# Performance work log

Hardware: AMD Instinct MI355X
Metric: run time of the kernel (lower is better)

Reference implementation:

```python
import jax, jax.numpy as jnp
import numpy as np


def _conv(x, w, b):
    # NCHW conv, 5x5, stride 1, SAME (pad 2)
    y = jax.lax.conv_general_dilated(x, w, (1, 1), 'SAME',
                                     dimension_numbers=('NCHW', 'OIHW', 'NCHW'))
    return y + b[None, :, None, None]


def _fwd(sequence_output, attention, adjacency, mention_idx, link_start, node_types, hts,
         W_trans, b_trans, type_embed, W_rel, W_self, b_rgcn,
         conv1_w, conv1_b, conv2_w, conv2_b, conv3_w, conv3_b,
         ht_W, ht_b, bil_W, bil_b):
    B, c, _ = sequence_output.shape
    E, M, LS = 22, 3, 16
    seq = sequence_output @ W_trans + b_trans              # [B,c,512] extractor_trans
    att_mean = attention.mean(1)                           # [B,c,c] head-averaged
    # ---- link nodes: attention-weighted span average (mean over heads, then matmul, then mean) ----
    pos = link_start[:, :, None] + jnp.arange(LS)          # [B,L,LS]
    fp = pos.reshape(B, -1)
    span = jnp.take_along_axis(seq, fp[:, :, None], axis=1).reshape(B, -1, LS, seq.shape[-1])
    rows = jnp.take_along_axis(att_mean, fp[:, :, None], axis=1).reshape(B, -1, LS, c)
    A = jnp.take_along_axis(rows, pos[:, :, None, :], axis=3)   # [B,L,LS,LS]
    link_nodes = jnp.einsum('blij,bljd->blid', A, span).mean(2)  # [B,L,512]
    # ---- mention gather + per-entity logsumexp pooling ----
    mf = mention_idx.reshape(B, -1)                              # [B,E*M]
    m_emb = jnp.take_along_axis(seq, mf[:, :, None], axis=1)     # [B,EM,512]
    entity_nodes = jax.nn.logsumexp(m_emb.reshape(B, E, M, -1), axis=2)   # [B,E,512]
    att_rows = jnp.take_along_axis(attention, mf[:, None, :, None], axis=2)  # [B,h,EM,c]
    entity_att = att_rows.reshape(B, att_rows.shape[1], E, M, c).mean(3)     # [B,h,E,c]
    # ---- assemble graph nodes + type embedding ----
    nodes = jnp.concatenate([entity_nodes, m_emb, link_nodes], axis=1)       # [B,N,512]
    nodes = jnp.concatenate([nodes, type_embed[node_types]], axis=-1)        # [B,N,532]
    # ---- 1-layer RGCN, 4 relations, row-normalized adjacency ----
    adj_n = adjacency / (adjacency.sum(-1, keepdims=True) + 1e-5)
    msg = jnp.einsum('brij,bjd->brid', adj_n, nodes)
    gcn = jax.nn.relu(jnp.einsum('brid,rdk->bik', msg, W_rel) + nodes @ W_self + b_rgcn)
    ent = gcn[:, :E]                                             # [B,E,512]
    # ---- entity context: normalized head-mean attention @ seq ----
    ea = entity_att.mean(1)
    ea = ea / (ea.sum(-1, keepdims=True) + 1e-5)
    e_ctx = jnp.einsum('bec,bcd->bed', ea, seq)                  # [B,E,512]
    # ---- per-channel outer-product relation maps ('ij,jk->jik') -> conv reasoning ----
    x = jnp.einsum('bid,bkd->bdik', ent, ent) + jnp.einsum('bid,bkd->bdik', e_ctx, e_ctx)
    x = jax.nn.relu(_conv(x, conv1_w, conv1_b))
    x = jax.nn.relu(_conv(x, conv2_w, conv2_b))
    x = jax.nn.relu(_conv(x, conv3_w, conv3_b))                  # [B,512,E,E]
    # ---- head/tail pair classification ----
    hi, ti = hts[..., 0], hts[..., 1]
    hs = jnp.take_along_axis(ent, hi[:, :, None], axis=1)
    ts = jnp.take_along_axis(ent, ti[:, :, None], axis=1)
    mflat = x.transpose(0, 2, 3, 1).reshape(B, E * E, -1)
    mfe = jnp.take_along_axis(mflat, (hi * E + ti)[:, :, None], axis=1)
    feat = jnp.concatenate([hs, ts, mfe, hs * ts], axis=-1)      # [B,P,2048]
    ht = jnp.tanh(feat @ ht_W + ht_b)                            # [B,P,1024]
    return ht @ bil_W + bil_b                                    # [B,P,97]


def setup_inputs() -> dict:
    key = jax.random.key(0)
    ks = jax.random.split(key, 16)
    B, c, H, h = 4, 1024, 768, 12
    E, M, L, N, P = 22, 3, 30, 118, 462
    emb, ic = 512, 256
    s = lambda k, sh: jax.random.normal(k, sh, jnp.float32) * 0.02
    inp = {}
    inp['sequence_output'] = jax.random.normal(ks[0], (B, c, H), jnp.float32)
    inp['attention'] = jax.random.uniform(ks[1], (B, h, c, c), dtype=jnp.float32)
    inp['adjacency'] = jax.random.uniform(ks[2], (B, 4, N, N), dtype=jnp.float32)
    inp['mention_idx'] = jax.random.randint(ks[3], (B, E, M), 0, c)
    inp['link_start'] = jax.random.randint(ks[4], (B, L), 0, c - 16)
    inp['node_types'] = jax.random.randint(ks[5], (B, N), 0, 3)
    inp['hts'] = jax.random.randint(ks[6], (B, P, 2), 0, E)
    inp['W_trans'] = s(ks[7], (H, emb)); inp['b_trans'] = jnp.zeros((emb,), jnp.float32)
    inp['type_embed'] = s(ks[8], (3, 20))
    inp['W_rel'] = s(ks[9], (4, emb + 20, emb))
    inp['W_self'] = s(ks[10], (emb + 20, emb)); inp['b_rgcn'] = jnp.zeros((emb,), jnp.float32)
    inp['conv1_w'] = s(ks[11], (ic, emb, 5, 5)); inp['conv1_b'] = jnp.zeros((ic,), jnp.float32)
    inp['conv2_w'] = s(ks[12], (ic, ic, 5, 5)); inp['conv2_b'] = jnp.zeros((ic,), jnp.float32)
    inp['conv3_w'] = s(ks[13], (emb, ic, 5, 5)); inp['conv3_b'] = jnp.zeros((emb,), jnp.float32)
    inp['ht_W'] = s(ks[14], (emb * 4, emb * 2)); inp['ht_b'] = jnp.zeros((emb * 2,), jnp.float32)
    inp['bil_W'] = s(ks[15], (emb * 2, 97)); inp['bil_b'] = jnp.zeros((97,), jnp.float32)
    return inp


def reference(sequence_output, attention, adjacency, mention_idx, link_start, node_types, hts,
              W_trans, b_trans, type_embed, W_rel, W_self, b_rgcn,
              conv1_w, conv1_b, conv2_w, conv2_b, conv3_w, conv3_b,
              ht_W, ht_b, bil_W, bil_b):
    return _fwd(sequence_output, attention, adjacency, mention_idx, link_start, node_types, hts,
                W_trans, b_trans, type_embed, W_rel, W_self, b_rgcn,
                conv1_w, conv1_b, conv2_w, conv2_b, conv3_w, conv3_b,
                ht_W, ht_b, bil_W, bil_b)
```

## Files before the change

### kernel.cpp

```cpp
#include <hip/hip_runtime.h>
#include <hip/hip_bf16.h>

constexpr int B   = 4;
constexpr int C   = 1024;
constexpr int HH  = 768;
constexpr int NHD = 12;
constexpr int E   = 22;
constexpr int MM  = 3;
constexpr int LL  = 30;
constexpr int NN  = 118;
constexpr int PP  = 462;
constexpr int EMB = 512;
constexpr int IC  = 256;
constexpr int LS  = 16;
constexpr int ND  = 532;
constexpr int KCAT = 4*ND + ND;


__global__ __launch_bounds__(256) void att_mean4_kernel(const float4* __restrict__ att,
                                                        float4* __restrict__ out) {
    int idx = blockIdx.x * 256 + threadIdx.x;
    int tot = B * C * C / 4;
    if (idx >= tot) return;
    int b = idx / (C * C / 4), rc = idx % (C * C / 4);
    const float4* p = att + (size_t)b * NHD * (C * C / 4) + rc;
    float sx = 0.f, sy = 0.f, sz = 0.f, sw = 0.f;
#pragma unroll
    for (int hh = 0; hh < NHD; hh++) {
        float4 v = p[(size_t)hh * (C * C / 4)];
        sx += v.x; sy += v.y; sz += v.z; sw += v.w;
    }
    const float inv = 1.0f / NHD;
    float4 r; r.x = sx * inv; r.y = sy * inv; r.z = sz * inv; r.w = sw * inv;
    out[idx] = r;
}

__global__ __launch_bounds__(256) void gemm_kernel(const float* __restrict__ A,
                                                   const float* __restrict__ Bm,
                                                   const float* __restrict__ bias,
                                                   float* __restrict__ Cc,
                                                   int M, int N, int K, int act) {
    __shared__ __align__(16) float As[16][68];
    __shared__ __align__(16) float Bs[16][68];
    int tid = threadIdx.x;
    int tx = tid & 15, ty = tid >> 4;
    int row0 = blockIdx.y * 64, col0 = blockIdx.x * 64;
    float acc[4][4] = {};
    for (int k0 = 0; k0 < K; k0 += 16) {
#pragma unroll
        for (int pass = 0; pass < 4; pass++) {
            int r = pass * 16 + (tid >> 4);
            int gr = row0 + r, gk = k0 + (tid & 15);
            As[tid & 15][r] = (gr < M && gk < K) ? A[(size_t)gr * K + gk] : 0.f;
        }
#pragma unroll
        for (int pass = 0; pass < 4; pass++) {
            int kk = pass * 4 + (tid >> 6);
            int cc = tid & 63;
            int gk = k0 + kk, gc = col0 + cc;
            Bs[kk][cc] = (gk < K && gc < N) ? Bm[(size_t)gk * N + gc] : 0.f;
        }
        __syncthreads();
#pragma unroll
        for (int kk = 0; kk < 16; kk++) {
            float4 av = *(const float4*)&As[kk][ty * 4];
            float4 bv = *(const float4*)&Bs[kk][tx * 4];
            float a[4] = {av.x, av.y, av.z, av.w};
            float bb[4] = {bv.x, bv.y, bv.z, bv.w};
#pragma unroll
            for (int i = 0; i < 4; i++)
#pragma unroll
                for (int j = 0; j < 4; j++) acc[i][j] += a[i] * bb[j];
        }
        __syncthreads();
    }
#pragma unroll
    for (int i = 0; i < 4; i++) {
        int gr = row0 + ty * 4 + i;
        if (gr >= M) continue;
#pragma unroll
        for (int j = 0; j < 4; j++) {
            int gc = col0 + tx * 4 + j;
            if (gc >= N) continue;
            float v = acc[i][j] + (bias ? bias[gc] : 0.f);
            if (act == 1) v = fmaxf(v, 0.f);
            else if (act == 2) v = tanhf(v);
            Cc[(size_t)gr * N + gc] = v;
        }
    }
}

__global__ __launch_bounds__(256) void gemm_splitk_kernel(const float* __restrict__ A,
                                                          const float* __restrict__ Bm,
                                                          float* __restrict__ part,
                                                          int M, int N, int K, int kb) {
    __shared__ __align__(16) float As[16][68];
    __shared__ __align__(16) float Bs[16][68];
    int z = blockIdx.z;
    int kbeg = z * kb;
    int kend = (kbeg + kb < K) ? (kbeg + kb) : K;
    int tid = threadIdx.x;
    int tx = tid & 15, ty = tid >> 4;
    int row0 = blockIdx.y * 64, col0 = blockIdx.x * 64;
    float acc[4][4] = {};
    for (int k0 = kbeg; k0 < kend; k0 += 16) {
#pragma unroll
        for (int pass = 0; pass < 4; pass++) {
            int r = pass * 16 + (tid >> 4);
            int gr = row0 + r, gk = k0 + (tid & 15);
            As[tid & 15][r] = (gr < M && gk < kend) ? A[(size_t)gr * K + gk] : 0.f;
        }
#pragma unroll
        for (int pass = 0; pass < 4; pass++) {
            int kk = pass * 4 + (tid >> 6);
            int cc = tid & 63;
            int gk = k0 + kk, gc = col0 + cc;
            Bs[kk][cc] = (gk < kend && gc < N) ? Bm[(size_t)gk * N + gc] : 0.f;
        }
        __syncthreads();
#pragma unroll
        for (int kk = 0; kk < 16; kk++) {
            float4 av = *(const float4*)&As[kk][ty * 4];
            float4 bv = *(const float4*)&Bs[kk][tx * 4];
            float a[4] = {av.x, av.y, av.z, av.w};
            float bb[4] = {bv.x, bv.y, bv.z, bv.w};
#pragma unroll
            for (int i = 0; i < 4; i++)
#pragma unroll
                for (int j = 0; j < 4; j++) acc[i][j] += a[i] * bb[j];
        }
        __syncthreads();
    }
    float* dst = part + (size_t)z * M * N;
#pragma unroll
    for (int i = 0; i < 4; i++) {
        int gr = row0 + ty * 4 + i;
        if (gr >= M) continue;
#pragma unroll
        for (int j = 0; j < 4; j++) {
            int gc = col0 + tx * 4 + j;
            if (gc >= N) continue;
            dst[(size_t)gr * N + gc] = acc[i][j];
        }
    }
}

__global__ __launch_bounds__(256) void reduce_sba_kernel(const float* __restrict__ part,
                                                         const float* __restrict__ bias,
                                                         float* __restrict__ out,
                                                         int MN, int N, int S, int act) {
    int idx = blockIdx.x * 256 + threadIdx.x;
    if (idx >= MN) return;
    float s = bias[idx % N];
    for (int z = 0; z < S; z++) s += part[(size_t)z * MN + idx];
    if (act == 1) s = fmaxf(s, 0.f);
    out[idx] = s;
}

__global__ __launch_bounds__(256) void gemmb_kernel(const float* __restrict__ A0,
                                                    const float* __restrict__ B0,
                                                    float* __restrict__ C0,
                                                    int M, int N, int K,
                                                    long sA, long sB, long sC) {
    const float* A = A0 + (size_t)blockIdx.z * sA;
    const float* Bm = B0 + (size_t)blockIdx.z * sB;
    float* Cc = C0 + (size_t)blockIdx.z * sC;
    __shared__ __align__(16) float As[16][68];
    __shared__ __align__(16) float Bs[16][68];
    int tid = threadIdx.x;
    int tx = tid & 15, ty = tid >> 4;
    int row0 = blockIdx.y * 64, col0 = blockIdx.x * 64;
    float acc[4][4] = {};
    for (int k0 = 0; k0 < K; k0 += 16) {
#pragma unroll
        for (int pass = 0; pass < 4; pass++) {
            int r = pass * 16 + (tid >> 4);
            int gr = row0 + r, gk = k0 + (tid & 15);
            As[tid & 15][r] = (gr < M && gk < K) ? A[(size_t)gr * K + gk] : 0.f;
        }
#pragma unroll
        for (int pass = 0; pass < 4; pass++) {
            int kk = pass * 4 + (tid >> 6);
            int cc = tid & 63;
            int gk = k0 + kk, gc = col0 + cc;
            Bs[kk][cc] = (gk < K && gc < N) ? Bm[(size_t)gk * N + gc] : 0.f;
        }
        __syncthreads();
#pragma unroll
        for (int kk = 0; kk < 16; kk++) {
            float4 av = *(const float4*)&As[kk][ty * 4];
            float4 bv = *(const float4*)&Bs[kk][tx * 4];
            float a[4] = {av.x, av.y, av.z, av.w};
            float bb[4] = {bv.x, bv.y, bv.z, bv.w};
#pragma unroll
            for (int i = 0; i < 4; i++)
#pragma unroll
                for (int j = 0; j < 4; j++) acc[i][j] += a[i] * bb[j];
        }
        __syncthreads();
    }
#pragma unroll
    for (int i = 0; i < 4; i++) {
        int gr = row0 + ty * 4 + i;
        if (gr >= M) continue;
#pragma unroll
        for (int j = 0; j < 4; j++) {
            int gc = col0 + tx * 4 + j;
            if (gc >= N) continue;
            Cc[(size_t)gr * N + gc] = acc[i][j];
        }
    }
}

__global__ __launch_bounds__(256) void nodes_fill_kernel(const float* __restrict__ seq,
                                                         const int* __restrict__ mention_idx,
                                                         const int* __restrict__ node_types,
                                                         const float* __restrict__ type_embed,
                                                         float* __restrict__ nodes) {
    int n = blockIdx.x, b = blockIdx.y, t = threadIdx.x;
    float* dst = nodes + ((size_t)b * NN + n) * ND;
    if (n < E) {
        const int* mi = mention_idx + (b * E + n) * MM;
        int i0 = mi[0], i1 = mi[1], i2 = mi[2];
        const float* s0 = seq + ((size_t)b * C + i0) * EMB;
        const float* s1 = seq + ((size_t)b * C + i1) * EMB;
        const float* s2 = seq + ((size_t)b * C + i2) * EMB;
        for (int d = t; d < EMB; d += 256) {
            float v0 = s0[d], v1 = s1[d], v2 = s2[d];
            float mx = fmaxf(v0, fmaxf(v1, v2));
            dst[d] = mx + logf(expf(v0 - mx) + expf(v1 - mx) + expf(v2 - mx));
        }
    } else if (n < E + E * MM) {
        int m = n - E;
        int src = mention_idx[b * E * MM + m];
        const float* sp = seq + ((size_t)b * C + src) * EMB;
        for (int d = t; d < EMB; d += 256) dst[d] = sp[d];
    }
    if (t < 20) {
        int ty_ = node_types[b * NN + n];
        dst[EMB + t] = type_embed[ty_ * 20 + t];
    }
}

__global__ __launch_bounds__(256) void link_nodes_kernel(const float* __restrict__ seq,
                                                         const float* __restrict__ am,
                                                         const int* __restrict__ link_start,
                                                         float* __restrict__ nodes) {
    int l = blockIdx.x, b = blockIdx.y, t = threadIdx.x;
    __shared__ float Ash[LS][LS];
    __shared__ float w[LS];
    int start = link_start[b * LL + l];
    {
        int i = t >> 4, j = t & 15;
        Ash[i][j] = am[((size_t)b * C + start + i) * C + (start + j)];
    }
    __syncthreads();
    if (t < LS) {
        float s = 0.f;
#pragma unroll
        for (int i = 0; i < LS; i++) s += Ash[i][t];
        w[t] = s * (1.0f / LS);
    }
    __syncthreads();
    float* dst = nodes + ((size_t)b * NN + (E + E * MM) + l) * ND;
    for (int d = t; d < EMB; d += 256) {
        float acc = 0.f;
#pragma unroll
        for (int j = 0; j < LS; j++) acc += w[j] * seq[((size_t)b * C + start + j) * EMB + d];
        dst[d] = acc;
    }
}

__global__ __launch_bounds__(256) void ea_kernel(const float* __restrict__ am,
                                                 const int* __restrict__ mention_idx,
                                                 float* __restrict__ ea) {
    int e = blockIdx.x, b = blockIdx.y, t = threadIdx.x;
    const int* mi = mention_idx + (b * E + e) * MM;
    int i0 = mi[0], i1 = mi[1], i2 = mi[2];
    const float* r0 = am + ((size_t)b * C + i0) * C;
    const float* r1 = am + ((size_t)b * C + i1) * C;
    const float* r2 = am + ((size_t)b * C + i2) * C;
    float* dst = ea + ((size_t)b * E + e) * C;
    __shared__ float red[256];
    float psum = 0.f;
    for (int ct = t; ct < C; ct += 256) {
        float v = (r0[ct] + r1[ct] + r2[ct]) * (1.0f / 3.0f);
        dst[ct] = v;
        psum += v;
    }
    red[t] = psum;
    __syncthreads();
    for (int s = 128; s > 0; s >>= 1) {
        if (t < s) red[t] += red[t + s];
        __syncthreads();
    }
    float inv = 1.0f / (red[0] + 1e-5f);
    for (int ct = t; ct < C; ct += 256) dst[ct] *= inv;
}

__global__ __launch_bounds__(128) void adjn_kernel(const float* __restrict__ adj,
                                                   float* __restrict__ adjn) {
    int row = blockIdx.x;
    int t = threadIdx.x;
    const float* src = adj + (size_t)row * NN;
    __shared__ float red[128];
    float s = (t < NN) ? src[t] : 0.f;
    red[t] = s;
    __syncthreads();
    for (int st = 64; st > 0; st >>= 1) {
        if (t < st) red[t] += red[t + st];
        __syncthreads();
    }
    float inv = 1.0f / (red[0] + 1e-5f);
    if (t < NN) adjn[(size_t)row * NN + t] = src[t] * inv;
}

__global__ __launch_bounds__(256) void msg_kernel(const float* __restrict__ adjn,
                                                  const float* __restrict__ nodes,
                                                  float* __restrict__ Arow) {
    int i = blockIdx.x, r = blockIdx.y, b = blockIdx.z;
    int t = threadIdx.x;
    __shared__ float a_sh[NN];
    if (t < NN) a_sh[t] = adjn[(((size_t)b * 4 + r) * NN + i) * NN + t];
    __syncthreads();
    float* dst = Arow + ((size_t)b * NN + i) * KCAT;
    const float* nb = nodes + (size_t)b * NN * ND;
    for (int d = t; d < ND; d += 256) {
        float acc = 0.f;
        for (int j = 0; j < NN; j++) acc += a_sh[j] * nb[(size_t)j * ND + d];
        dst[r * ND + d] = acc;
        if (r == 0) dst[4 * ND + d] = nb[(size_t)i * ND + d];
    }
}

__global__ __launch_bounds__(512) void pairwise_kernel(const float* __restrict__ gcn,
                                                       const float* __restrict__ ectx,
                                                       float* __restrict__ x) {
    int d = blockIdx.x, b = blockIdx.y, t = threadIdx.x;
    __shared__ float ev[E], cv[E];
    if (t < E) ev[t] = gcn[((size_t)b * NN + t) * EMB + d];
    else if (t < 2 * E) cv[t - E] = ectx[((size_t)b * E + (t - E)) * EMB + d];
    __syncthreads();
    if (t < E * E) {
        int i = t / E, k = t % E;
        x[((size_t)b * EMB + d) * (E * E) + t] = ev[i] * ev[k] + cv[i] * cv[k];
    }
}

__global__ __launch_bounds__(256) void conv5k_kernel(const float* __restrict__ in,
                                                     const float* __restrict__ w,
                                                     float* __restrict__ part,
                                                     int Cin, int Cout, int CH) {
    constexpr int G = 2;
    int nch = Cin / CH;
    int z = blockIdx.z;
    int b = z / nch, ch = z - b * nch;
    int co0 = blockIdx.x * 64;
    int r0 = blockIdx.y * 8;
    int t = threadIdx.x;
    int tx = t & 15, ty = t >> 4;

    __shared__ __align__(16) float As[G * 25 * 68];
    __shared__ __align__(16) float Pl[G * 12 * 28];

    int qr[3], qc[3];
#pragma unroll
    for (int s = 0; s < 3; s++) {
        int q = tx + s * 16;
        qr[s] = q / 6;
        qc[s] = (q - qr[s] * 6) * 4;
    }

    float acc[3][4][4] = {};

    const float* inb = in + ((size_t)b * Cin + ch * CH) * 484;
    const float* wb  = w + ((size_t)co0 * Cin + (size_t)ch * CH) * 25;

    for (int c0 = 0; c0 < CH; c0 += G) {
        __syncthreads();
        for (int idx = t; idx < G * 336; idx += 256) {
            int g = idx / 336, rem = idx - g * 336;
            int r = rem / 28, c = rem - r * 28;
            int ih = r0 - 2 + r, iw = c - 2;
            float v = 0.f;
            if (ih >= 0 && ih < 22 && iw >= 0 && iw < 22)
                v = inb[(size_t)(c0 + g) * 484 + ih * 22 + iw];
            Pl[(g * 12 + r) * 28 + c] = v;
        }
        for (int idx = t; idx < G * 1600; idx += 256) {
            int g = idx / 1600, rem = idx - g * 1600;
            int co = rem / 25, tap = rem - co * 25;
            As[(g * 25 + tap) * 68 + co] = wb[(size_t)co * Cin * 25 + (size_t)(c0 + g) * 25 + tap];
        }
        __syncthreads();
#pragma unroll
        for (int g = 0; g < G; g++) {
            const float* plg = &Pl[g * 336];
            const float* asg = &As[g * 1700];
#pragma unroll
            for (int dy = 0; dy < 5; dy++) {
                float iv[3][8];
#pragma unroll
                for (int s = 0; s < 3; s++) {
                    float4 v0 = *(const float4*)&plg[(qr[s] + dy) * 28 + qc[s]];
                    float4 v1 = *(const float4*)&plg[(qr[s] + dy) * 28 + qc[s] + 4];
                    iv[s][0] = v0.x; iv[s][1] = v0.y; iv[s][2] = v0.z; iv[s][3] = v0.w;
                    iv[s][4] = v1.x; iv[s][5] = v1.y; iv[s][6] = v1.z; iv[s][7] = v1.w;
                }
#pragma unroll
                for (int dx = 0; dx < 5; dx++) {
                    float4 wv = *(const float4*)&asg[(dy * 5 + dx) * 68 + ty * 4];
                    float wf[4] = {wv.x, wv.y, wv.z, wv.w};
#pragma unroll
                    for (int s = 0; s < 3; s++)
#pragma unroll
                        for (int i = 0; i < 4; i++)
#pragma unroll
                            for (int j = 0; j < 4; j++)
                                acc[s][i][j] += wf[i] * iv[s][dx + j];
                }
            }
        }
    }
    float* dst0 = part + ((size_t)z * Cout + co0 + ty * 4) * 484;
#pragma unroll
    for (int s = 0; s < 3; s++) {
        int row = r0 + qr[s];
        if (row >= 22) continue;
#pragma unroll
        for (int i = 0; i < 4; i++) {
            float* dr = dst0 + (size_t)i * 484 + row * 22;
#pragma unroll
            for (int j = 0; j < 4; j++) {
                int col = qc[s] + j;
                if (col < 22) dr[col] = acc[s][i][j];
            }
        }
    }
}

__global__ __launch_bounds__(256) void reduce_bias_relu_kernel(const float* __restrict__ part,
                                                               const float* __restrict__ bias,
                                                               float* __restrict__ out,
                                                               int Cout, int nch) {
    int idx = blockIdx.x * 256 + threadIdx.x;
    int total = B * Cout * 484;
    if (idx >= total) return;
    int b = idx / (Cout * 484);
    int rem = idx % (Cout * 484);
    int co = rem / 484;
    float s = bias[co];
    const float* p = part + ((size_t)b * nch) * Cout * 484 + rem;
    for (int ch = 0; ch < nch; ch++) s += p[(size_t)ch * Cout * 484];
    out[idx] = fmaxf(s, 0.f);
}

__global__ __launch_bounds__(256) void reduce3_transpose_kernel(const float* __restrict__ part,
                                                                const float* __restrict__ bias,
                                                                float* __restrict__ mflat,
                                                                int nch) {
    __shared__ float tl[32][33];
    int b = blockIdx.z;
    int co0 = blockIdx.x * 32, pp0 = blockIdx.y * 32;
    int tx = threadIdx.x % 32, tyy = threadIdx.x / 32;
    for (int i = tyy; i < 32; i += 8) {
        int co = co0 + i, p = pp0 + tx;
        float v = 0.f;
        if (p < 484) {
            v = bias[co];
            const float* src = part + (((size_t)b * nch) * 512 + co) * 484 + p;
            for (int ch = 0; ch < nch; ch++) v += src[(size_t)ch * 512 * 484];
            v = fmaxf(v, 0.f);
        }
        tl[i][tx] = v;
    }
    __syncthreads();
    for (int i = tyy; i < 32; i += 8) {
        int p = pp0 + i, co = co0 + tx;
        if (p < 484) mflat[((size_t)b * 484 + p) * 512 + co] = tl[tx][i];
    }
}

__global__ __launch_bounds__(256) void feat_kernel(const float* __restrict__ gcn,
                                                   const float* __restrict__ mflat,
                                                   const int* __restrict__ hts,
                                                   float* __restrict__ feat) {
    int p = blockIdx.x, b = blockIdx.y, t = threadIdx.x;
    int hi = hts[((size_t)b * PP + p) * 2];
    int ti = hts[((size_t)b * PP + p) * 2 + 1];
    const float* hsrc = gcn + ((size_t)b * NN + hi) * EMB;
    const float* tsrc = gcn + ((size_t)b * NN + ti) * EMB;
    const float* msrc = mflat + ((size_t)b * 484 + hi * E + ti) * EMB;
    float* dst = feat + ((size_t)b * PP + p) * (4 * EMB);
    for (int d = t; d < EMB; d += 256) {
        float hv = hsrc[d], tv = tsrc[d];
        dst[d] = hv;
        dst[EMB + d] = tv;
        dst[2 * EMB + d] = msrc[d];
        dst[3 * EMB + d] = hv * tv;
    }
}

extern "C" void kernel_launch(void* const* d_in, const int* in_sizes, int n_in,
                              void* d_out, int out_size, void* d_ws, size_t ws_size,
                              hipStream_t stream) {
    const float* sequence_output = (const float*)d_in[0];
    const float* attention      = (const float*)d_in[1];
    const float* adjacency      = (const float*)d_in[2];
    const int*   mention_idx    = (const int*)d_in[3];
    const int*   link_start     = (const int*)d_in[4];
    const int*   node_types     = (const int*)d_in[5];
    const int*   hts            = (const int*)d_in[6];
    const float* W_trans        = (const float*)d_in[7];
    const float* b_trans        = (const float*)d_in[8];
    const float* type_embed     = (const float*)d_in[9];
    const float* W_rel          = (const float*)d_in[10];
    const float* W_self         = (const float*)d_in[11];
    const float* b_rgcn         = (const float*)d_in[12];
    const float* conv1_w        = (const float*)d_in[13];
    const float* conv1_b        = (const float*)d_in[14];
    const float* conv2_w        = (const float*)d_in[15];
    const float* conv2_b        = (const float*)d_in[16];
    const float* conv3_w        = (const float*)d_in[17];
    const float* conv3_b        = (const float*)d_in[18];
    const float* ht_W           = (const float*)d_in[19];
    const float* ht_b           = (const float*)d_in[20];
    const float* bil_W          = (const float*)d_in[21];
    const float* bil_b          = (const float*)d_in[22];
    float* out = (float*)d_out;
    float* ws = (float*)d_ws;

    float* att_mean = ws;
    float* Arow    = ws;
    float* Bcat    = ws + 1255520;
    float* gcnpart = ws + 2617440;
    float* xbuf    = ws;
    float* y1      = ws + 991232;
    float* y2      = ws + 1486848;
    float* part    = ws + 1982464;
    float* seqb    = ws + 4194304;
    float* ea      = ws + 6291456;
    float* mflat   = ws;
    float* feat    = ws + 991232;
    float* htbuf   = ws + 4800000;
    float* nodes   = ws + 9912320;
    float* adjn    = ws + 10163424;
    float* ectx    = ws + 10386208;
    float* gcnb    = ws + 10431264;

    att_mean4_kernel<<<(B * C * C / 4 + 255) / 256, 256, 0, stream>>>(
        (const float4*)attention, (float4*)att_mean);
    gemm_kernel<<<dim3(EMB / 64, (B * C) / 64), 256, 0, stream>>>(
        sequence_output, W_trans, b_trans, seqb, B * C, EMB, HH, 0);
    nodes_fill_kernel<<<dim3(NN, B), 256, 0, stream>>>(seqb, mention_idx, node_types,
                                                       type_embed, nodes);
    link_nodes_kernel<<<dim3(LL, B), 256, 0, stream>>>(seqb, att_mean, link_start, nodes);
    ea_kernel<<<dim3(E, B), 256, 0, stream>>>(att_mean, mention_idx, ea);
    gemmb_kernel<<<dim3(EMB / 64, 1, B), 256, 0, stream>>>(
        ea, seqb, ectx, E, EMB, C, (long)E * C, (long)C * EMB, (long)E * EMB);
    adjn_kernel<<<B * 4 * NN, 128, 0, stream>>>(adjacency, adjn);
    msg_kernel<<<dim3(NN, 4, B), 256, 0, stream>>>(adjn, nodes, Arow);
    hipMemcpyAsync(Bcat, W_rel, (size_t)4 * ND * EMB * sizeof(float),
                   hipMemcpyDeviceToDevice, stream);
    hipMemcpyAsync(Bcat + (size_t)4 * ND * EMB, W_self, (size_t)ND * EMB * sizeof(float),
                   hipMemcpyDeviceToDevice, stream);
    gemm_splitk_kernel<<<dim3(8, 8, 4), 256, 0, stream>>>(Arow, Bcat, gcnpart,
                                                          B * NN, EMB, KCAT, 672);
    reduce_sba_kernel<<<(B * NN * EMB + 255) / 256, 256, 0, stream>>>(
        gcnpart, b_rgcn, gcnb, B * NN * EMB, EMB, 4, 1);
    pairwise_kernel<<<dim3(EMB, B), 512, 0, stream>>>(gcnb, ectx, xbuf);
    conv5k_kernel<<<dim3(4, 3, B * 16), 256, 0, stream>>>(xbuf, conv1_w, part, 512, 256, 32);
    reduce_bias_relu_kernel<<<(B * 256 * 484 + 255) / 256, 256, 0, stream>>>(
        part, conv1_b, y1, 256, 16);
    conv5k_kernel<<<dim3(4, 3, B * 16), 256, 0, stream>>>(y1, conv2_w, part, 256, 256, 16);
    reduce_bias_relu_kernel<<<(B * 256 * 484 + 255) / 256, 256, 0, stream>>>(
        part, conv2_b, y2, 256, 16);
    conv5k_kernel<<<dim3(8, 3, B * 8), 256, 0, stream>>>(y2, conv3_w, part, 256, 512, 32);
    reduce3_transpose_kernel<<<dim3(16, 16, B), 256, 0, stream>>>(part, conv3_b, mflat, 8);
    feat_kernel<<<dim3(PP, B), 256, 0, stream>>>(gcnb, mflat, hts, feat);
    gemm_kernel<<<dim3(16, 29), 256, 0, stream>>>(feat, ht_W, ht_b, htbuf, B * PP, 1024,
                                                  2048, 2);
    gemm_kernel<<<dim3(2, 29), 256, 0, stream>>>(htbuf, bil_W, bil_b, out, B * PP, 97,
                                                 1024, 0);
}
```

Before: 2.240 ms.

## Run ht projection GEMM on bf16 MFMA with transposed bf16 weights

Casts the pair feature matrix to bf16 as it is built and transposes and converts ht_W to bf16 every call. The 1848x1024x2048 ht GEMM then runs on a new MFMA 16x16x32 bf16 kernel instead of the fp32 SIMT tiled GEMM. This is meant to cut the compute time of that GEMM and halve the bytes of its operands, at the cost of bf16 rounding error and an extra per-call transpose kernel.

```diff
diff --git a/kernel.cpp b/kernel.cpp
--- a/kernel.cpp
+++ b/kernel.cpp
@@ -15,6 +15,9 @@
 constexpr int LS  = 16;
 constexpr int ND  = 532;
 constexpr int KCAT = 4*ND + ND;
+
+typedef __attribute__((ext_vector_type(8))) short bf16x8;
+typedef __attribute__((ext_vector_type(4))) float f32x4;
 
 
 __global__ __launch_bounds__(256) void att_mean4_kernel(const float4* __restrict__ att,
@@ -208,6 +211,69 @@
             int gc = col0 + tx * 4 + j;
             if (gc >= N) continue;
             Cc[(size_t)gr * N + gc] = acc[i][j];
+        }
+    }
+}
+
+__global__ __launch_bounds__(256) void transpose_bf16_kernel(const float* __restrict__ W,
+                                                             __hip_bfloat16* __restrict__ Wt,
+                                                             int K, int N) {
+    __shared__ float tl[32][33];
+    int k0 = blockIdx.x * 32, n0 = blockIdx.y * 32;
+    int tx = threadIdx.x & 31, ty = threadIdx.x >> 5;
+    for (int i = ty; i < 32; i += 8) {
+        int k = k0 + i, n = n0 + tx;
+        tl[i][tx] = (k < K && n < N) ? W[(size_t)k * N + n] : 0.f;
+    }
+    __syncthreads();
+    for (int i = ty; i < 32; i += 8) {
+        int n = n0 + i, k = k0 + tx;
+        if (n < N && k < K) Wt[(size_t)n * K + k] = __float2bfloat16(tl[tx][i]);
+    }
+}
+
+__global__ __launch_bounds__(256) void gemm_mfma_kernel(const __hip_bfloat16* __restrict__ A,
+                                                        const __hip_bfloat16* __restrict__ Bt,
+                                                        const float* __restrict__ bias,
+                                                        float* __restrict__ Cc,
+                                                        int M, int N, int K, int act) {
+    __shared__ __align__(16) short Asub[4 * 64 * 8];
+    __shared__ __align__(16) short Bsub[4 * 64 * 8];
+    int t = threadIdx.x;
+    int row0 = blockIdx.y * 64, col0 = blockIdx.x * 64;
+    int w = t >> 6, l = t & 63;
+    int r = t >> 2, kh = t & 3;
+    f32x4 acc[4] = {};
+    for (int k0 = 0; k0 < K; k0 += 32) {
+        __syncthreads();
+        {
+            int gr = row0 + r;
+            uint4 va = make_uint4(0u, 0u, 0u, 0u);
+            if (gr < M) va = *(const uint4*)&A[(size_t)gr * K + k0 + kh * 8];
+            *(uint4*)&Asub[(kh * 64 + r) * 8] = va;
+            uint4 vb = *(const uint4*)&Bt[(size_t)(col0 + r) * K + k0 + kh * 8];
+            *(uint4*)&Bsub[(kh * 64 + r) * 8] = vb;
+        }
+        __syncthreads();
+        bf16x8 a = *(const bf16x8*)&Asub[((l >> 4) * 64 + w * 16 + (l & 15)) * 8];
+#pragma unroll
+        for (int n = 0; n < 4; n++) {
+            bf16x8 b = *(const bf16x8*)&Bsub[((l >> 4) * 64 + n * 16 + (l & 15)) * 8];
+            acc[n] = __builtin_amdgcn_mfma_f32_16x16x32_bf16(a, b, acc[n], 0, 0, 0);
+        }
+    }
+#pragma unroll
+    for (int n = 0; n < 4; n++) {
+        int col = col0 + n * 16 + (l & 15);
+        if (col >= N) continue;
+#pragma unroll
+        for (int i = 0; i < 4; i++) {
+            int row = row0 + w * 16 + (l >> 4) * 4 + i;
+            if (row >= M) continue;
+            float v = acc[n][i] + (bias ? bias[col] : 0.f);
+            if (act == 1) v = fmaxf(v, 0.f);
+            else if (act == 2) v = tanhf(v);
+            Cc[(size_t)row * N + col] = v;
         }
     }
 }
@@ -481,23 +547,23 @@
     }
 }
 
-__global__ __launch_bounds__(256) void feat_kernel(const float* __restrict__ gcn,
-                                                   const float* __restrict__ mflat,
-                                                   const int* __restrict__ hts,
-                                                   float* __restrict__ feat) {
+__global__ __launch_bounds__(256) void feat_bf16_kernel(const float* __restrict__ gcn,
+                                                        const float* __restrict__ mflat,
+                                                        const int* __restrict__ hts,
+                                                        __hip_bfloat16* __restrict__ feat) {
     int p = blockIdx.x, b = blockIdx.y, t = threadIdx.x;
     int hi = hts[((size_t)b * PP + p) * 2];
     int ti = hts[((size_t)b * PP + p) * 2 + 1];
     const float* hsrc = gcn + ((size_t)b * NN + hi) * EMB;
     const float* tsrc = gcn + ((size_t)b * NN + ti) * EMB;
     const float* msrc = mflat + ((size_t)b * 484 + hi * E + ti) * EMB;
-    float* dst = feat + ((size_t)b * PP + p) * (4 * EMB);
+    __hip_bfloat16* dst = feat + ((size_t)b * PP + p) * (4 * EMB);
     for (int d = t; d < EMB; d += 256) {
         float hv = hsrc[d], tv = tsrc[d];
-        dst[d] = hv;
-        dst[EMB + d] = tv;
-        dst[2 * EMB + d] = msrc[d];
-        dst[3 * EMB + d] = hv * tv;
+        dst[d] = __float2bfloat16(hv);
+        dst[EMB + d] = __float2bfloat16(tv);
+        dst[2 * EMB + d] = __float2bfloat16(msrc[d]);
+        dst[3 * EMB + d] = __float2bfloat16(hv * tv);
     }
 }
 
@@ -541,7 +607,8 @@
     float* seqb    = ws + 4194304;
     float* ea      = ws + 6291456;
     float* mflat   = ws;
-    float* feat    = ws + 991232;
+    __hip_bfloat16* featb = (__hip_bfloat16*)(ws + 991232);
+    __hip_bfloat16* htWt  = (__hip_bfloat16*)(ws + 2883584);
     float* htbuf   = ws + 4800000;
     float* nodes   = ws + 9912320;
     float* adjn    = ws + 10163424;
@@ -577,9 +644,11 @@
         part, conv2_b, y2, 256, 16);
     conv5k_kernel<<<dim3(8, 3, B * 8), 256, 0, stream>>>(y2, conv3_w, part, 256, 512, 32);
     reduce3_transpose_kernel<<<dim3(16, 16, B), 256, 0, stream>>>(part, conv3_b, mflat, 8);
-    feat_kernel<<<dim3(PP, B), 256, 0, stream>>>(gcnb, mflat, hts, feat);
-    gemm_kernel<<<dim3(16, 29), 256, 0, stream>>>(feat, ht_W, ht_b, htbuf, B * PP, 1024,
-                                                  2048, 2);
+    feat_bf16_kernel<<<dim3(PP, B), 256, 0, stream>>>(gcnb, mflat, hts, featb);
+    transpose_bf16_kernel<<<dim3(2048 / 32, 1024 / 32), 256, 0, stream>>>(ht_W, htWt,
+                                                                          2048, 1024);
+    gemm_mfma_kernel<<<dim3(16, 29), 256, 0, stream>>>(featb, htWt, ht_b, htbuf,
+                                                       B * PP, 1024, 2048, 2);
     gemm_kernel<<<dim3(2, 29), 256, 0, stream>>>(htbuf, bil_W, bil_b, out, B * PP, 97,
                                                  1024, 0);
 }
```

New measurement: 1.890 ms. 1.19x faster.
